# Kernel optimization log

Measured on AMD Instinct MI355X. Metric: run time of the kernel, lower is better.

Reference implementation:

```python
import jax, jax.numpy as jnp
import numpy as np

# Haar (db1) filters after the index reversals done in create_wavelet_filter.
_S = np.float32(1.0 / np.sqrt(2.0))
_LO = np.array([_S, _S], np.float32)
_HI = np.array([_S, -_S], np.float32)
# dec[k, i, j]; band order: LL, (hi rows)*lo, lo*(hi cols), HH -> matches torch stack order
_DEC = np.stack([np.outer(_LO, _LO), np.outer(_HI, _LO), np.outer(_LO, _HI), np.outer(_HI, _HI)], 0)
_REC = _DEC  # identical for Haar


def dwt(x):
    # non-overlapping 2x2 stride-2 depthwise conv == blocked einsum
    b, c, h, w = x.shape
    xr = x.reshape(b, c, h // 2, 2, w // 2, 2)
    return jnp.einsum('bcipjq,kpq->bckij', xr, jnp.asarray(_DEC))  # [b,c,4,h/2,w/2]


def idwt(x):
    # stride-2 kernel-2 transposed depthwise conv == blocked einsum
    b, c, _, h, w = x.shape
    y = jnp.einsum('bckij,kpq->bcipjq', x, jnp.asarray(_REC))
    return y.reshape(b, c, 2 * h, 2 * w)


def dwconv3(x, w, bias=None):
    # depthwise 3x3 'same' conv; w: [C,1,3,3]
    c = x.shape[1]
    y = jax.lax.conv_general_dilated(x, w, (1, 1), 'SAME', feature_group_count=c,
                                     dimension_numbers=('NCHW', 'OIHW', 'NCHW'))
    if bias is not None:
        y = y + bias[None, :, None, None]
    return y


def setup_inputs() -> dict:
    key = jax.random.key(0)
    ks = jax.random.split(key, 8)
    B, C, H, W = 16, 64, 256, 256
    inp = {
        'x': jax.random.normal(ks[0], (B, C, H, W), jnp.float32),
        'base_w': jax.random.normal(ks[1], (C, 1, 3, 3), jnp.float32) * 0.1,
        'base_b': jax.random.normal(ks[2], (C,), jnp.float32) * 0.01,
        'base_scale': jnp.ones((1, C, 1, 1), jnp.float32),
        'ww0': jax.random.normal(ks[3], (4 * C, 1, 3, 3), jnp.float32) * 0.1,
        'ww1': jax.random.normal(ks[4], (4 * C, 1, 3, 3), jnp.float32) * 0.1,
        'ww2': jax.random.normal(ks[5], (4 * C, 1, 3, 3), jnp.float32) * 0.1,
        'ws0': jnp.full((1, 4 * C, 1, 1), 0.1, jnp.float32),
        'ws1': jnp.full((1, 4 * C, 1, 1), 0.1, jnp.float32),
        'ws2': jnp.full((1, 4 * C, 1, 1), 0.1, jnp.float32),
        'gamma': jnp.ones((C,), jnp.float32),
        'beta': jnp.zeros((C,), jnp.float32),
    }
    return inp


def reference(x, base_w, base_b, base_scale, ww0, ww1, ww2, ws0, ws1, ws2, gamma, beta):
    wws = [ww0, ww1, ww2]
    wss = [ws0, ws1, ws2]
    levels = 3
    lls, hs = [], []
    cur = x
    # --- WTConv2d: recursive wavelet pyramid (H,W divisible by 2**levels, no odd-pad) ---
    for i in range(levels):
        cx = dwt(cur)                # [b,c,4,h/2,w/2]
        cur = cx[:, :, 0]            # LL feeds next level
        b_, c_, _, h_, w_ = cx.shape
        t = cx.reshape(b_, c_ * 4, h_, w_)
        t = dwconv3(t, wws[i]) * wss[i]   # depthwise conv (no bias) + learned scale
        t = t.reshape(b_, c_, 4, h_, w_)
        lls.append(t[:, :, 0])
        hs.append(t[:, :, 1:4])
    nxt = jnp.zeros_like(lls[-1])
    for i in range(levels - 1, -1, -1):
        ll = lls[i] + nxt
        cx = jnp.concatenate([ll[:, :, None], hs[i]], axis=2)
        nxt = idwt(cx)
    # base depthwise conv path
    y = dwconv3(x, base_w, base_b) * base_scale + nxt
    # --- BatchNorm2d (training-mode batch stats, eps=1e-5) + ReLU ---
    mean = y.mean(axis=(0, 2, 3), keepdims=True)
    var = ((y - mean) ** 2).mean(axis=(0, 2, 3), keepdims=True)
    y = (y - mean) * jax.lax.rsqrt(var + 1e-5)
    y = y * gamma[None, :, None, None] + beta[None, :, None, None]
    return jax.nn.relu(y)
```

## Files before the change

### kernel.cpp

```cpp
#include <hip/hip_runtime.h>
#include <hip/hip_bf16.h>

#define NB 16
#define NC 64

static __device__ __forceinline__ unsigned short f2bfr(float f) {
    union { float f; unsigned u; } cv; cv.f = f;
    unsigned r = cv.u + 0x7fffu + ((cv.u >> 16) & 1u);
    return (unsigned short)(r >> 16);
}
static __device__ __forceinline__ float bfr2f(unsigned short h) {
    union { unsigned u; float f; } cv; cv.u = ((unsigned)h) << 16;
    return cv.f;
}

template <int H>
static __device__ __forceinline__ void stage_tile(
    const float* __restrict__ src, size_t ibase, int sTop, int sLeft,
    float (*sIn)[72], int tid)
{
#pragma unroll
    for (int i = 0; i < 5; ++i) {
        int idx = i * 256 + tid;
        if (idx < 68 * 16) {
            int r = idx >> 4, c4 = (idx & 15) << 2;
            int gy = sTop + r, gx = sLeft + c4;
            float4 v = make_float4(0.f, 0.f, 0.f, 0.f);
            if ((unsigned)gy < (unsigned)H && (unsigned)gx < (unsigned)H)
                v = *(const float4*)(src + ibase + (size_t)gy * H + gx);
            *(float4*)(&sIn[r][c4]) = v;
        }
    }
    if (tid < 136) {
        int r = tid >> 1, c4 = 64 + ((tid & 1) << 2);
        int gy = sTop + r, gx = sLeft + c4;
        float4 v = make_float4(0.f, 0.f, 0.f, 0.f);
        if ((unsigned)gy < (unsigned)H && (unsigned)gx < (unsigned)H)
            v = *(const float4*)(src + ibase + (size_t)gy * H + gx);
        *(float4*)(&sIn[r][c4]) = v;
    }
}

__global__ __launch_bounds__(256) void ll_kernel(
    const float* __restrict__ in, float* __restrict__ ll)
{
    int t = blockIdx.x * 256 + threadIdx.x;
    int jp  = t & 63;
    int i   = (t >> 6) & 127;
    int img = t >> 13;
    size_t ib = (size_t)img * 65536;
    float4 a = *(const float4*)(in + ib + (size_t)(2 * i) * 256 + 4 * jp);
    float4 b = *(const float4*)(in + ib + (size_t)(2 * i + 1) * 256 + 4 * jp);
    float2 o;
    o.x = 0.5f * (a.x + a.y + b.x + b.y);
    o.y = 0.5f * (a.z + a.w + b.z + b.w);
    *(float2*)(ll + (size_t)img * 16384 + (size_t)i * 128 + 2 * jp) = o;
}

template <int H>
__global__ __launch_bounds__(256) void dwt_conv_kernel(
    const float* __restrict__ in, const float* __restrict__ ww,
    const float* __restrict__ wsc, float* __restrict__ t_out,
    float* __restrict__ curn)
{
    constexpr int H2 = H / 2;
    constexpr int TX = H2 / 32;
    const int tile = blockIdx.x;
    const int c = blockIdx.y, b = blockIdx.z;
    const int ty = tile / TX, tx = tile % TX;
    const int oy0 = ty * 32, ox0 = tx * 32;
    const int tid = threadIdx.x;

    __shared__ float sIn[68][72];

    float w[4][9], sc[4];
#pragma unroll
    for (int k = 0; k < 4; ++k) {
#pragma unroll
        for (int i = 0; i < 9; ++i) w[k][i] = ww[(c * 4 + k) * 9 + i];
        sc[k] = 0.5f * wsc[c * 4 + k];
    }

    const size_t ibase = (size_t)(b * NC + c) * H * H;
    stage_tile<H>(in, ibase, 2 * oy0 - 2, 2 * ox0 - 4, sIn, tid);
    __syncthreads();

    const size_t tbase = (size_t)(b * NC + c) * 4 * H2 * H2;
    const size_t cbase = (size_t)(b * NC + c) * H2 * H2;
    const int qj = tid & 31;
    const int qi0 = tid >> 5;
#pragma unroll
    for (int it = 0; it < 4; ++it) {
        int qi = qi0 + 8 * it;
        float P[6][6];
#pragma unroll
        for (int r = 0; r < 6; ++r) {
            const float2* rp = (const float2*)&sIn[2 * qi + r][2 * qj + 2];
            float2 p0 = rp[0], p1 = rp[1], p2 = rp[2];
            P[r][0] = p0.x; P[r][1] = p0.y; P[r][2] = p1.x;
            P[r][3] = p1.y; P[r][4] = p2.x; P[r][5] = p2.y;
        }
        float kk0 = 0.f, kk1 = 0.f, kk2 = 0.f, kk3 = 0.f, llc = 0.f;
#pragma unroll
        for (int r = 0; r < 3; ++r)
#pragma unroll
            for (int s = 0; s < 3; ++s) {
                float a = P[2*r][2*s],   e = P[2*r][2*s+1];
                float f = P[2*r+1][2*s], g = P[2*r+1][2*s+1];
                float s0 = a + e, s1 = f + g, d0 = a - e, d1 = f - g;
                float b0 = s0 + s1;
                kk0 += w[0][3*r+s] * b0;
                kk1 += w[1][3*r+s] * (s0 - s1);
                kk2 += w[2][3*r+s] * (d0 + d1);
                kk3 += w[3][3*r+s] * (d0 - d1);
                if (r == 1 && s == 1) llc = 0.5f * b0;
            }
        size_t o = (size_t)(oy0 + qi) * H2 + (ox0 + qj);
        t_out[tbase + o]                       = kk0 * sc[0];
        t_out[tbase + (size_t)H2 * H2 + o]     = kk1 * sc[1];
        t_out[tbase + (size_t)2 * H2 * H2 + o] = kk2 * sc[2];
        t_out[tbase + (size_t)3 * H2 * H2 + o] = kk3 * sc[3];
        if (curn) curn[cbase + o] = llc;
    }
}

__global__ __launch_bounds__(256) void idwt_fuse_kernel(
    const float* __restrict__ t1, const float* __restrict__ t2,
    float* __restrict__ nxt1)
{
    int idx = blockIdx.x * 256 + threadIdx.x;
    int j = idx & 63, i = (idx >> 6) & 63, img = idx >> 12;
    size_t t2b = (size_t)img * 4096 + (size_t)(i >> 1) * 32 + (j >> 1);
    float m0 = t2[t2b], m1 = t2[t2b + 1024], m2 = t2[t2b + 2048], m3 = t2[t2b + 3072];
    float a1 = (i & 1) ? -m1 : m1;
    float a2 = (j & 1) ? -m2 : m2;
    float a3 = ((i ^ j) & 1) ? -m3 : m3;
    float nxt2v = 0.5f * (m0 + a1 + a2 + a3);
    size_t t1b = (size_t)img * 16384 + (size_t)i * 64 + j;
    float k0 = t1[t1b] + nxt2v;
    float k1 = t1[t1b + 4096], k2 = t1[t1b + 8192], k3 = t1[t1b + 12288];
    size_t ob = (size_t)img * 16384 + (size_t)(2 * i) * 128 + 2 * j;
    *(float2*)(nxt1 + ob) = make_float2(0.5f * (k0 + k1 + k2 + k3),
                                        0.5f * (k0 + k1 - k2 - k3));
    *(float2*)(nxt1 + ob + 128) = make_float2(0.5f * (k0 - k1 + k2 - k3),
                                              0.5f * (k0 - k1 - k2 + k3));
}

__global__ __launch_bounds__(256) void final_fuse_kernel(
    const float* __restrict__ x, const float* __restrict__ nxt1,
    const float* __restrict__ bw, const float* __restrict__ bb,
    const float* __restrict__ bs, const float* __restrict__ ww0,
    const float* __restrict__ ws0,
    unsigned short* __restrict__ ybf, float2* __restrict__ partials)
{
    const int tile = blockIdx.x, c = blockIdx.y, b = blockIdx.z;
    const int ty = tile >> 2, tx = tile & 3;
    const int oy0 = ty * 64, ox0 = tx * 64;
    const int hy0 = ty * 32, hx0 = tx * 32;
    const int tid = threadIdx.x;

    __shared__ float sIn[68][72];
    __shared__ float rS[256], rQ[256];

    float w[4][9], sc[4], wb[9];
#pragma unroll
    for (int k = 0; k < 4; ++k) {
#pragma unroll
        for (int i = 0; i < 9; ++i) w[k][i] = ww0[(c * 4 + k) * 9 + i];
        sc[k] = 0.25f * ws0[c * 4 + k];
    }
#pragma unroll
    for (int i = 0; i < 9; ++i) wb[i] = bw[c * 9 + i];
    const float scale = bs[c];
    const float bsc = bb[c] * scale;

    const size_t xb = (size_t)(b * NC + c) * 65536;
    stage_tile<256>(x, xb, oy0 - 2, ox0 - 4, sIn, tid);
    __syncthreads();

    const size_t n1b = (size_t)(b * NC + c) * 16384;
    const int qj = tid & 31;
    const int qi0 = tid >> 5;
    float lsum = 0.f, lss = 0.f;
#pragma unroll
    for (int it = 0; it < 4; ++it) {
        int qi = qi0 + 8 * it;
        float P[6][6];
#pragma unroll
        for (int r = 0; r < 6; ++r) {
            const float2* rp = (const float2*)&sIn[2 * qi + r][2 * qj + 2];
            float2 p0 = rp[0], p1 = rp[1], p2 = rp[2];
            P[r][0] = p0.x; P[r][1] = p0.y; P[r][2] = p1.x;
            P[r][3] = p1.y; P[r][4] = p2.x; P[r][5] = p2.y;
        }
        float kk0 = 0.f, kk1 = 0.f, kk2 = 0.f, kk3 = 0.f;
#pragma unroll
        for (int r = 0; r < 3; ++r)
#pragma unroll
            for (int s = 0; s < 3; ++s) {
                float a = P[2*r][2*s],   e = P[2*r][2*s+1];
                float f = P[2*r+1][2*s], g = P[2*r+1][2*s+1];
                float s0 = a + e, s1 = f + g, d0 = a - e, d1 = f - g;
                kk0 += w[0][3*r+s] * (s0 + s1);
                kk1 += w[1][3*r+s] * (s0 - s1);
                kk2 += w[2][3*r+s] * (d0 + d1);
                kk3 += w[3][3*r+s] * (d0 - d1);
            }
        kk0 = kk0 * sc[0] + 0.5f * nxt1[n1b + (size_t)(hy0 + qi) * 128 + (hx0 + qj)];
        kk1 *= sc[1];
        kk2 *= sc[2];
        kk3 *= sc[3];
        float vv[2][2];
        vv[0][0] = kk0 + kk1 + kk2 + kk3;
        vv[0][1] = kk0 + kk1 - kk2 - kk3;
        vv[1][0] = kk0 - kk1 + kk2 - kk3;
        vv[1][1] = kk0 - kk1 - kk2 + kk3;
        int yl = 2 * qi, xl = 2 * qj;
#pragma unroll
        for (int p = 0; p < 2; ++p) {
            unsigned pack = 0;
#pragma unroll
            for (int q = 0; q < 2; ++q) {
                float acc = 0.f;
#pragma unroll
                for (int r = 0; r < 3; ++r)
#pragma unroll
                    for (int s = 0; s < 3; ++s)
                        acc += P[p + r + 1][q + s + 1] * wb[3 * r + s];
                float val = fmaf(acc, scale, bsc) + vv[p][q];
                lsum += val;
                lss = fmaf(val, val, lss);
                pack |= ((unsigned)f2bfr(val)) << (16 * q);
            }
            *(unsigned*)(ybf + xb + (size_t)(oy0 + yl + p) * 256 + (ox0 + xl)) = pack;
        }
    }
    rS[tid] = lsum;
    rQ[tid] = lss;
    __syncthreads();
    for (int off = 128; off > 0; off >>= 1) {
        if (tid < off) { rS[tid] += rS[tid + off]; rQ[tid] += rQ[tid + off]; }
        __syncthreads();
    }
    if (tid == 0)
        partials[c * 256 + b * 16 + tile] = make_float2(rS[0], rQ[0]);
}

__global__ __launch_bounds__(256) void stats_kernel(
    const float2* __restrict__ partials, const float* __restrict__ gamma,
    const float* __restrict__ beta, float2* __restrict__ ab)
{
    const int c = blockIdx.x;
    const int tid = threadIdx.x;
    __shared__ float s1[256], s2[256];
    float2 p = partials[c * 256 + tid];
    s1[tid] = p.x;
    s2[tid] = p.y;
    __syncthreads();
    for (int off = 128; off > 0; off >>= 1) {
        if (tid < off) { s1[tid] += s1[tid + off]; s2[tid] += s2[tid + off]; }
        __syncthreads();
    }
    if (tid == 0) {
        const float N = (float)NB * 65536.0f;
        float mean = s1[0] / N;
        float var = s2[0] / N - mean * mean;
        float inv = rsqrtf(var + 1e-5f);
        float a = gamma[c] * inv;
        ab[c] = make_float2(a, beta[c] - mean * a);
    }
}

__global__ __launch_bounds__(256) void norm_out_kernel(
    const unsigned short* __restrict__ ybf, const float2* __restrict__ ab,
    float* __restrict__ out)
{
    const long total8 = (long)NB * NC * 65536 / 8;
    const long stride = (long)gridDim.x * 256;
    for (long i = blockIdx.x * 256L + threadIdx.x; i < total8; i += stride) {
        long e = i * 8;
        int c = (int)((e >> 16) & (NC - 1));
        float2 s = ab[c];
        uint4 v = *(const uint4*)(ybf + e);
        float4 o0, o1;
        o0.x = fmaxf(fmaf(bfr2f((unsigned short)(v.x & 0xffff)), s.x, s.y), 0.f);
        o0.y = fmaxf(fmaf(bfr2f((unsigned short)(v.x >> 16)),    s.x, s.y), 0.f);
        o0.z = fmaxf(fmaf(bfr2f((unsigned short)(v.y & 0xffff)), s.x, s.y), 0.f);
        o0.w = fmaxf(fmaf(bfr2f((unsigned short)(v.y >> 16)),    s.x, s.y), 0.f);
        o1.x = fmaxf(fmaf(bfr2f((unsigned short)(v.z & 0xffff)), s.x, s.y), 0.f);
        o1.y = fmaxf(fmaf(bfr2f((unsigned short)(v.z >> 16)),    s.x, s.y), 0.f);
        o1.z = fmaxf(fmaf(bfr2f((unsigned short)(v.w & 0xffff)), s.x, s.y), 0.f);
        o1.w = fmaxf(fmaf(bfr2f((unsigned short)(v.w >> 16)),    s.x, s.y), 0.f);
        *(float4*)(out + e) = o0;
        *(float4*)(out + e + 4) = o1;
    }
}

extern "C" void kernel_launch(void* const* d_in, const int* in_sizes, int n_in,
                              void* d_out, int out_size, void* d_ws, size_t ws_size,
                              hipStream_t stream)
{
    const float* x    = (const float*)d_in[0];
    const float* bw   = (const float*)d_in[1];
    const float* bb   = (const float*)d_in[2];
    const float* bs   = (const float*)d_in[3];
    const float* ww0  = (const float*)d_in[4];
    const float* ww1  = (const float*)d_in[5];
    const float* ww2  = (const float*)d_in[6];
    const float* ws0  = (const float*)d_in[7];
    const float* ws1  = (const float*)d_in[8];
    const float* ws2  = (const float*)d_in[9];
    const float* gamma = (const float*)d_in[10];
    const float* beta  = (const float*)d_in[11];

    char* w = (char*)d_ws;
    float* cur1 = (float*)(w);
    float* t1   = (float*)(w + 67108864);
    float* cur2 = (float*)(w + 67108864 + 67108864);
    float* t2   = (float*)(w + 67108864 + 83886080);
    unsigned short* ybf = (unsigned short*)(w + 67108864);
    float2* partials = (float2*)(w + 67108864 + 134217728);
    float2* ab       = (float2*)(w + 67108864 + 134217728 + 131072);
    float* nxt1 = cur1;

    ll_kernel<<<dim3(NB * NC * 128 * 64 / 256), 256, 0, stream>>>(x, cur1);
    dwt_conv_kernel<128><<<dim3(4, NC, NB), 256, 0, stream>>>(cur1, ww1, ws1, t1, cur2);
    dwt_conv_kernel<64><<<dim3(1, NC, NB), 256, 0, stream>>>(cur2, ww2, ws2, t2, nullptr);
    idwt_fuse_kernel<<<dim3(NB * NC * 4096 / 256), 256, 0, stream>>>(t1, t2, nxt1);
    final_fuse_kernel<<<dim3(16, NC, NB), 256, 0, stream>>>(x, nxt1, bw, bb, bs, ww0, ws0, ybf, partials);
    stats_kernel<<<dim3(64), 256, 0, stream>>>(partials, gamma, beta, ab);
    norm_out_kernel<<<dim3(2048), 256, 0, stream>>>(ybf, ab, (float*)d_out);
}
```

Before: 363.6 us.

## Fuse idwt into final kernel, store wavelet bands as bf16, 2x2 register blocking

```diff
diff --git a/kernel.cpp b/kernel.cpp
--- a/kernel.cpp
+++ b/kernel.cpp
@@ -13,11 +13,14 @@
     union { unsigned u; float f; } cv; cv.u = ((unsigned)h) << 16;
     return cv.f;
 }
+static __device__ __forceinline__ unsigned pack2bf(float lo, float hi) {
+    return ((unsigned)f2bfr(lo)) | (((unsigned)f2bfr(hi)) << 16);
+}
 
 template <int H>
 static __device__ __forceinline__ void stage_tile(
     const float* __restrict__ src, size_t ibase, int sTop, int sLeft,
-    float (*sIn)[72], int tid)
+    float (*sIn)[76], int tid)
 {
 #pragma unroll
     for (int i = 0; i < 5; ++i) {
@@ -60,7 +63,7 @@
 template <int H>
 __global__ __launch_bounds__(256) void dwt_conv_kernel(
     const float* __restrict__ in, const float* __restrict__ ww,
-    const float* __restrict__ wsc, float* __restrict__ t_out,
+    const float* __restrict__ wsc, unsigned short* __restrict__ t_out,
     float* __restrict__ curn)
 {
     constexpr int H2 = H / 2;
@@ -70,8 +73,9 @@
     const int ty = tile / TX, tx = tile % TX;
     const int oy0 = ty * 32, ox0 = tx * 32;
     const int tid = threadIdx.x;
-
-    __shared__ float sIn[68][72];
+    const int qi = 2 * (tid >> 4), qj = 2 * (tid & 15);
+
+    __shared__ float sIn[68][76];
 
     float w[4][9], sc[4];
 #pragma unroll
@@ -85,81 +89,87 @@
     stage_tile<H>(in, ibase, 2 * oy0 - 2, 2 * ox0 - 4, sIn, tid);
     __syncthreads();
 
+    float kk[4][4];
+#pragma unroll
+    for (int i = 0; i < 4; ++i)
+#pragma unroll
+        for (int j = 0; j < 4; ++j) kk[i][j] = 0.f;
+    float llc[4];
+
+    const int pr0 = 2 * qi, pc0 = 2 * qj + 2;
+#pragma unroll
+    for (int rp = 0; rp < 4; ++rp) {
+        float xa[8], xb[8];
+#pragma unroll
+        for (int n = 0; n < 4; ++n) {
+            float2 va = *(const float2*)&sIn[pr0 + 2 * rp][pc0 + 2 * n];
+            float2 vb = *(const float2*)&sIn[pr0 + 2 * rp + 1][pc0 + 2 * n];
+            xa[2 * n] = va.x; xa[2 * n + 1] = va.y;
+            xb[2 * n] = vb.x; xb[2 * n + 1] = vb.y;
+        }
+        float D0[4], D1[4], D2[4], D3[4];
+#pragma unroll
+        for (int n = 0; n < 4; ++n) {
+            float a = xa[2 * n], e = xa[2 * n + 1];
+            float f = xb[2 * n], g = xb[2 * n + 1];
+            float s0 = a + e, s1 = f + g, d0 = a - e, d1 = f - g;
+            D0[n] = s0 + s1; D1[n] = s0 - s1;
+            D2[n] = d0 + d1; D3[n] = d0 - d1;
+        }
+#pragma unroll
+        for (int mi = 0; mi < 2; ++mi) {
+            const int r = rp - mi;
+            if (r >= 0 && r <= 2) {
+#pragma unroll
+                for (int mj = 0; mj < 2; ++mj) {
+                    const int m = 2 * mi + mj;
+#pragma unroll
+                    for (int s = 0; s < 3; ++s) {
+                        kk[0][m] = fmaf(w[0][3 * r + s], D0[mj + s], kk[0][m]);
+                        kk[1][m] = fmaf(w[1][3 * r + s], D1[mj + s], kk[1][m]);
+                        kk[2][m] = fmaf(w[2][3 * r + s], D2[mj + s], kk[2][m]);
+                        kk[3][m] = fmaf(w[3][3 * r + s], D3[mj + s], kk[3][m]);
+                    }
+                }
+                if (r == 1) {
+                    llc[2 * mi + 0] = 0.5f * D0[1];
+                    llc[2 * mi + 1] = 0.5f * D0[2];
+                }
+            }
+        }
+    }
+
     const size_t tbase = (size_t)(b * NC + c) * 4 * H2 * H2;
-    const size_t cbase = (size_t)(b * NC + c) * H2 * H2;
-    const int qj = tid & 31;
-    const int qi0 = tid >> 5;
-#pragma unroll
-    for (int it = 0; it < 4; ++it) {
-        int qi = qi0 + 8 * it;
-        float P[6][6];
-#pragma unroll
-        for (int r = 0; r < 6; ++r) {
-            const float2* rp = (const float2*)&sIn[2 * qi + r][2 * qj + 2];
-            float2 p0 = rp[0], p1 = rp[1], p2 = rp[2];
-            P[r][0] = p0.x; P[r][1] = p0.y; P[r][2] = p1.x;
-            P[r][3] = p1.y; P[r][4] = p2.x; P[r][5] = p2.y;
-        }
-        float kk0 = 0.f, kk1 = 0.f, kk2 = 0.f, kk3 = 0.f, llc = 0.f;
-#pragma unroll
-        for (int r = 0; r < 3; ++r)
-#pragma unroll
-            for (int s = 0; s < 3; ++s) {
-                float a = P[2*r][2*s],   e = P[2*r][2*s+1];
-                float f = P[2*r+1][2*s], g = P[2*r+1][2*s+1];
-                float s0 = a + e, s1 = f + g, d0 = a - e, d1 = f - g;
-                float b0 = s0 + s1;
-                kk0 += w[0][3*r+s] * b0;
-                kk1 += w[1][3*r+s] * (s0 - s1);
-                kk2 += w[2][3*r+s] * (d0 + d1);
-                kk3 += w[3][3*r+s] * (d0 - d1);
-                if (r == 1 && s == 1) llc = 0.5f * b0;
-            }
-        size_t o = (size_t)(oy0 + qi) * H2 + (ox0 + qj);
-        t_out[tbase + o]                       = kk0 * sc[0];
-        t_out[tbase + (size_t)H2 * H2 + o]     = kk1 * sc[1];
-        t_out[tbase + (size_t)2 * H2 * H2 + o] = kk2 * sc[2];
-        t_out[tbase + (size_t)3 * H2 * H2 + o] = kk3 * sc[3];
-        if (curn) curn[cbase + o] = llc;
-    }
-}
-
-__global__ __launch_bounds__(256) void idwt_fuse_kernel(
-    const float* __restrict__ t1, const float* __restrict__ t2,
-    float* __restrict__ nxt1)
-{
-    int idx = blockIdx.x * 256 + threadIdx.x;
-    int j = idx & 63, i = (idx >> 6) & 63, img = idx >> 12;
-    size_t t2b = (size_t)img * 4096 + (size_t)(i >> 1) * 32 + (j >> 1);
-    float m0 = t2[t2b], m1 = t2[t2b + 1024], m2 = t2[t2b + 2048], m3 = t2[t2b + 3072];
-    float a1 = (i & 1) ? -m1 : m1;
-    float a2 = (j & 1) ? -m2 : m2;
-    float a3 = ((i ^ j) & 1) ? -m3 : m3;
-    float nxt2v = 0.5f * (m0 + a1 + a2 + a3);
-    size_t t1b = (size_t)img * 16384 + (size_t)i * 64 + j;
-    float k0 = t1[t1b] + nxt2v;
-    float k1 = t1[t1b + 4096], k2 = t1[t1b + 8192], k3 = t1[t1b + 12288];
-    size_t ob = (size_t)img * 16384 + (size_t)(2 * i) * 128 + 2 * j;
-    *(float2*)(nxt1 + ob) = make_float2(0.5f * (k0 + k1 + k2 + k3),
-                                        0.5f * (k0 + k1 - k2 - k3));
-    *(float2*)(nxt1 + ob + 128) = make_float2(0.5f * (k0 - k1 + k2 - k3),
-                                              0.5f * (k0 - k1 - k2 + k3));
+    const size_t o00 = (size_t)(oy0 + qi) * H2 + (ox0 + qj);
+#pragma unroll
+    for (int band = 0; band < 4; ++band) {
+        size_t bo = tbase + (size_t)band * H2 * H2 + o00;
+#pragma unroll
+        for (int mi = 0; mi < 2; ++mi)
+            *(unsigned*)(t_out + bo + (size_t)mi * H2) =
+                pack2bf(kk[band][2 * mi] * sc[band], kk[band][2 * mi + 1] * sc[band]);
+    }
+    if (curn) {
+        const size_t cbase = (size_t)(b * NC + c) * H2 * H2 + o00;
+        *(float2*)(curn + cbase)      = make_float2(llc[0], llc[1]);
+        *(float2*)(curn + cbase + H2) = make_float2(llc[2], llc[3]);
+    }
 }
 
 __global__ __launch_bounds__(256) void final_fuse_kernel(
-    const float* __restrict__ x, const float* __restrict__ nxt1,
-    const float* __restrict__ bw, const float* __restrict__ bb,
-    const float* __restrict__ bs, const float* __restrict__ ww0,
-    const float* __restrict__ ws0,
+    const float* __restrict__ x, const unsigned short* __restrict__ t1,
+    const unsigned short* __restrict__ t2, const float* __restrict__ bw,
+    const float* __restrict__ bb, const float* __restrict__ bs,
+    const float* __restrict__ ww0, const float* __restrict__ ws0,
     unsigned short* __restrict__ ybf, float2* __restrict__ partials)
 {
     const int tile = blockIdx.x, c = blockIdx.y, b = blockIdx.z;
     const int ty = tile >> 2, tx = tile & 3;
     const int oy0 = ty * 64, ox0 = tx * 64;
-    const int hy0 = ty * 32, hx0 = tx * 32;
     const int tid = threadIdx.x;
-
-    __shared__ float sIn[68][72];
+    const int qi = 2 * (tid >> 4), qj = 2 * (tid & 15);
+
+    __shared__ float sIn[68][76];
     __shared__ float rS[256], rQ[256];
 
     float w[4][9], sc[4], wb[9];
@@ -176,65 +186,134 @@
 
     const size_t xb = (size_t)(b * NC + c) * 65536;
     stage_tile<256>(x, xb, oy0 - 2, ox0 - 4, sIn, tid);
+
+    const int i1 = ty * 16 + (tid >> 4);
+    const int j1 = tx * 16 + (tid & 15);
+    const size_t img = (size_t)(b * NC + c);
+    const size_t t1b = img * 16384 + (size_t)i1 * 64 + j1;
+    const size_t t2b = img * 4096 + (size_t)(i1 >> 1) * 32 + (j1 >> 1);
+    float m0 = bfr2f(t2[t2b]);
+    float m1 = bfr2f(t2[t2b + 1024]);
+    float m2 = bfr2f(t2[t2b + 2048]);
+    float m3 = bfr2f(t2[t2b + 3072]);
+    float a1 = (i1 & 1) ? -m1 : m1;
+    float a2 = (j1 & 1) ? -m2 : m2;
+    float a3 = ((i1 ^ j1) & 1) ? -m3 : m3;
+    float k0 = bfr2f(t1[t1b]) + 0.5f * (m0 + a1 + a2 + a3);
+    float k1 = bfr2f(t1[t1b + 4096]);
+    float k2 = bfr2f(t1[t1b + 8192]);
+    float k3 = bfr2f(t1[t1b + 12288]);
+    float nxtq[2][2];
+    nxtq[0][0] = 0.25f * (k0 + k1 + k2 + k3);
+    nxtq[0][1] = 0.25f * (k0 + k1 - k2 - k3);
+    nxtq[1][0] = 0.25f * (k0 - k1 + k2 - k3);
+    nxtq[1][1] = 0.25f * (k0 - k1 - k2 + k3);
+
     __syncthreads();
 
-    const size_t n1b = (size_t)(b * NC + c) * 16384;
-    const int qj = tid & 31;
-    const int qi0 = tid >> 5;
+    float kk[4][4];
+#pragma unroll
+    for (int i = 0; i < 4; ++i)
+#pragma unroll
+        for (int j = 0; j < 4; ++j) kk[i][j] = 0.f;
+    float acc[4][4];
+#pragma unroll
+    for (int i = 0; i < 4; ++i)
+#pragma unroll
+        for (int j = 0; j < 4; ++j) acc[i][j] = 0.f;
+
+    const int pr0 = 2 * qi, pc0 = 2 * qj + 2;
+#pragma unroll
+    for (int rp = 0; rp < 4; ++rp) {
+        float xa[8], xb8[8];
+#pragma unroll
+        for (int n = 0; n < 4; ++n) {
+            float2 va = *(const float2*)&sIn[pr0 + 2 * rp][pc0 + 2 * n];
+            float2 vb = *(const float2*)&sIn[pr0 + 2 * rp + 1][pc0 + 2 * n];
+            xa[2 * n] = va.x; xa[2 * n + 1] = va.y;
+            xb8[2 * n] = vb.x; xb8[2 * n + 1] = vb.y;
+        }
+        float D0[4], D1[4], D2[4], D3[4];
+#pragma unroll
+        for (int n = 0; n < 4; ++n) {
+            float a = xa[2 * n], e = xa[2 * n + 1];
+            float f = xb8[2 * n], g = xb8[2 * n + 1];
+            float s0 = a + e, s1 = f + g, d0 = a - e, d1 = f - g;
+            D0[n] = s0 + s1; D1[n] = s0 - s1;
+            D2[n] = d0 + d1; D3[n] = d0 - d1;
+        }
+#pragma unroll
+        for (int mi = 0; mi < 2; ++mi) {
+            const int r = rp - mi;
+            if (r >= 0 && r <= 2) {
+#pragma unroll
+                for (int mj = 0; mj < 2; ++mj) {
+                    const int m = 2 * mi + mj;
+#pragma unroll
+                    for (int s = 0; s < 3; ++s) {
+                        kk[0][m] = fmaf(w[0][3 * r + s], D0[mj + s], kk[0][m]);
+                        kk[1][m] = fmaf(w[1][3 * r + s], D1[mj + s], kk[1][m]);
+                        kk[2][m] = fmaf(w[2][3 * r + s], D2[mj + s], kk[2][m]);
+                        kk[3][m] = fmaf(w[3][3 * r + s], D3[mj + s], kk[3][m]);
+                    }
+                }
+            }
+        }
+#pragma unroll
+        for (int half = 0; half < 2; ++half) {
+            const int kr = 2 * rp + half;
+#pragma unroll
+            for (int p = 0; p < 4; ++p) {
+                const int rr = kr - 1 - p;
+                if (rr >= 0 && rr < 3) {
+#pragma unroll
+                    for (int u = 0; u < 4; ++u) {
+                        float t = half ? (xb8[u + 1] * wb[3 * rr] +
+                                          xb8[u + 2] * wb[3 * rr + 1] +
+                                          xb8[u + 3] * wb[3 * rr + 2])
+                                       : (xa[u + 1] * wb[3 * rr] +
+                                          xa[u + 2] * wb[3 * rr + 1] +
+                                          xa[u + 3] * wb[3 * rr + 2]);
+                        acc[p][u] += t;
+                    }
+                }
+            }
+        }
+    }
+
+    float val[4][4];
     float lsum = 0.f, lss = 0.f;
 #pragma unroll
-    for (int it = 0; it < 4; ++it) {
-        int qi = qi0 + 8 * it;
-        float P[6][6];
-#pragma unroll
-        for (int r = 0; r < 6; ++r) {
-            const float2* rp = (const float2*)&sIn[2 * qi + r][2 * qj + 2];
-            float2 p0 = rp[0], p1 = rp[1], p2 = rp[2];
-            P[r][0] = p0.x; P[r][1] = p0.y; P[r][2] = p1.x;
-            P[r][3] = p1.y; P[r][4] = p2.x; P[r][5] = p2.y;
-        }
-        float kk0 = 0.f, kk1 = 0.f, kk2 = 0.f, kk3 = 0.f;
-#pragma unroll
-        for (int r = 0; r < 3; ++r)
-#pragma unroll
-            for (int s = 0; s < 3; ++s) {
-                float a = P[2*r][2*s],   e = P[2*r][2*s+1];
-                float f = P[2*r+1][2*s], g = P[2*r+1][2*s+1];
-                float s0 = a + e, s1 = f + g, d0 = a - e, d1 = f - g;
-                kk0 += w[0][3*r+s] * (s0 + s1);
-                kk1 += w[1][3*r+s] * (s0 - s1);
-                kk2 += w[2][3*r+s] * (d0 + d1);
-                kk3 += w[3][3*r+s] * (d0 - d1);
-            }
-        kk0 = kk0 * sc[0] + 0.5f * nxt1[n1b + (size_t)(hy0 + qi) * 128 + (hx0 + qj)];
-        kk1 *= sc[1];
-        kk2 *= sc[2];
-        kk3 *= sc[3];
-        float vv[2][2];
-        vv[0][0] = kk0 + kk1 + kk2 + kk3;
-        vv[0][1] = kk0 + kk1 - kk2 - kk3;
-        vv[1][0] = kk0 - kk1 + kk2 - kk3;
-        vv[1][1] = kk0 - kk1 - kk2 + kk3;
-        int yl = 2 * qi, xl = 2 * qj;
-#pragma unroll
-        for (int p = 0; p < 2; ++p) {
-            unsigned pack = 0;
-#pragma unroll
-            for (int q = 0; q < 2; ++q) {
-                float acc = 0.f;
-#pragma unroll
-                for (int r = 0; r < 3; ++r)
-#pragma unroll
-                    for (int s = 0; s < 3; ++s)
-                        acc += P[p + r + 1][q + s + 1] * wb[3 * r + s];
-                float val = fmaf(acc, scale, bsc) + vv[p][q];
-                lsum += val;
-                lss = fmaf(val, val, lss);
-                pack |= ((unsigned)f2bfr(val)) << (16 * q);
-            }
-            *(unsigned*)(ybf + xb + (size_t)(oy0 + yl + p) * 256 + (ox0 + xl)) = pack;
-        }
-    }
+    for (int mi = 0; mi < 2; ++mi)
+#pragma unroll
+        for (int mj = 0; mj < 2; ++mj) {
+            const int m = 2 * mi + mj;
+            float c0 = fmaf(kk[0][m], sc[0], nxtq[mi][mj]);
+            float c1 = kk[1][m] * sc[1];
+            float c2 = kk[2][m] * sc[2];
+            float c3 = kk[3][m] * sc[3];
+            float vv00 = c0 + c1 + c2 + c3;
+            float vv01 = c0 + c1 - c2 - c3;
+            float vv10 = c0 - c1 + c2 - c3;
+            float vv11 = c0 - c1 - c2 + c3;
+            val[2 * mi + 0][2 * mj + 0] = fmaf(acc[2 * mi + 0][2 * mj + 0], scale, bsc) + vv00;
+            val[2 * mi + 0][2 * mj + 1] = fmaf(acc[2 * mi + 0][2 * mj + 1], scale, bsc) + vv01;
+            val[2 * mi + 1][2 * mj + 0] = fmaf(acc[2 * mi + 1][2 * mj + 0], scale, bsc) + vv10;
+            val[2 * mi + 1][2 * mj + 1] = fmaf(acc[2 * mi + 1][2 * mj + 1], scale, bsc) + vv11;
+        }
+#pragma unroll
+    for (int p = 0; p < 4; ++p) {
+#pragma unroll
+        for (int u = 0; u < 4; ++u) {
+            lsum += val[p][u];
+            lss = fmaf(val[p][u], val[p][u], lss);
+        }
+        uint2 st;
+        st.x = pack2bf(val[p][0], val[p][1]);
+        st.y = pack2bf(val[p][2], val[p][3]);
+        *(uint2*)(ybf + xb + (size_t)(oy0 + 2 * qi + p) * 256 + (ox0 + 2 * qj)) = st;
+    }
+
     rS[tid] = lsum;
     rQ[tid] = lss;
     __syncthreads();
@@ -314,20 +393,18 @@
     const float* beta  = (const float*)d_in[11];
 
     char* w = (char*)d_ws;
-    float* cur1 = (float*)(w);
-    float* t1   = (float*)(w + 67108864);
-    float* cur2 = (float*)(w + 67108864 + 67108864);
-    float* t2   = (float*)(w + 67108864 + 83886080);
-    unsigned short* ybf = (unsigned short*)(w + 67108864);
-    float2* partials = (float2*)(w + 67108864 + 134217728);
-    float2* ab       = (float2*)(w + 67108864 + 134217728 + 131072);
-    float* nxt1 = cur1;
+    unsigned short* ybf = (unsigned short*)(w);
+    float*          cur1 = (float*)(w);
+    unsigned short* t1   = (unsigned short*)(w + 134217728);
+    float*          cur2 = (float*)(w + 167772160);
+    unsigned short* t2   = (unsigned short*)(w + 184549376);
+    float2*         partials = (float2*)(w + 192937984);
+    float2*         ab       = (float2*)(w + 193069056);
 
     ll_kernel<<<dim3(NB * NC * 128 * 64 / 256), 256, 0, stream>>>(x, cur1);
     dwt_conv_kernel<128><<<dim3(4, NC, NB), 256, 0, stream>>>(cur1, ww1, ws1, t1, cur2);
     dwt_conv_kernel<64><<<dim3(1, NC, NB), 256, 0, stream>>>(cur2, ww2, ws2, t2, nullptr);
-    idwt_fuse_kernel<<<dim3(NB * NC * 4096 / 256), 256, 0, stream>>>(t1, t2, nxt1);
-    final_fuse_kernel<<<dim3(16, NC, NB), 256, 0, stream>>>(x, nxt1, bw, bb, bs, ww0, ws0, ybf, partials);
+    final_fuse_kernel<<<dim3(16, NC, NB), 256, 0, stream>>>(x, t1, t2, bw, bb, bs, ww0, ws0, ybf, partials);
     stats_kernel<<<dim3(64), 256, 0, stream>>>(partials, gamma, beta, ab);
     norm_out_kernel<<<dim3(2048), 256, 0, stream>>>(ybf, ab, (float*)d_out);
 }
```

After: 411.2 us. +13.1%, slower.

## Store wavelet intermediates in bf16 and compute 2x2 outputs per thread

Applied to the files above, without the earlier changes.

```diff
diff --git a/kernel.cpp b/kernel.cpp
--- a/kernel.cpp
+++ b/kernel.cpp
@@ -13,11 +13,14 @@
     union { unsigned u; float f; } cv; cv.u = ((unsigned)h) << 16;
     return cv.f;
 }
+static __device__ __forceinline__ unsigned pack2bf(float lo, float hi) {
+    return ((unsigned)f2bfr(lo)) | (((unsigned)f2bfr(hi)) << 16);
+}
 
 template <int H>
 static __device__ __forceinline__ void stage_tile(
     const float* __restrict__ src, size_t ibase, int sTop, int sLeft,
-    float (*sIn)[72], int tid)
+    float (*sIn)[76], int tid)
 {
 #pragma unroll
     for (int i = 0; i < 5; ++i) {
@@ -60,7 +63,7 @@
 template <int H>
 __global__ __launch_bounds__(256) void dwt_conv_kernel(
     const float* __restrict__ in, const float* __restrict__ ww,
-    const float* __restrict__ wsc, float* __restrict__ t_out,
+    const float* __restrict__ wsc, unsigned short* __restrict__ t_out,
     float* __restrict__ curn)
 {
     constexpr int H2 = H / 2;
@@ -70,8 +73,9 @@
     const int ty = tile / TX, tx = tile % TX;
     const int oy0 = ty * 32, ox0 = tx * 32;
     const int tid = threadIdx.x;
-
-    __shared__ float sIn[68][72];
+    const int qi = 2 * (tid >> 4), qj = 2 * (tid & 15);
+
+    __shared__ float sIn[68][76];
 
     float w[4][9], sc[4];
 #pragma unroll
@@ -85,69 +89,102 @@
     stage_tile<H>(in, ibase, 2 * oy0 - 2, 2 * ox0 - 4, sIn, tid);
     __syncthreads();
 
+    float kk[4][4];
+#pragma unroll
+    for (int i = 0; i < 4; ++i)
+#pragma unroll
+        for (int j = 0; j < 4; ++j) kk[i][j] = 0.f;
+    float llc[4];
+
+    const int pr0 = 2 * qi, pc0 = 2 * qj + 2;
+#pragma unroll
+    for (int rp = 0; rp < 4; ++rp) {
+        float xa[8], xb[8];
+#pragma unroll
+        for (int n = 0; n < 4; ++n) {
+            float2 va = *(const float2*)&sIn[pr0 + 2 * rp][pc0 + 2 * n];
+            float2 vb = *(const float2*)&sIn[pr0 + 2 * rp + 1][pc0 + 2 * n];
+            xa[2 * n] = va.x; xa[2 * n + 1] = va.y;
+            xb[2 * n] = vb.x; xb[2 * n + 1] = vb.y;
+        }
+        float D0[4], D1[4], D2[4], D3[4];
+#pragma unroll
+        for (int n = 0; n < 4; ++n) {
+            float a = xa[2 * n], e = xa[2 * n + 1];
+            float f = xb[2 * n], g = xb[2 * n + 1];
+            float s0 = a + e, s1 = f + g, d0 = a - e, d1 = f - g;
+            D0[n] = s0 + s1; D1[n] = s0 - s1;
+            D2[n] = d0 + d1; D3[n] = d0 - d1;
+        }
+#pragma unroll
+        for (int mi = 0; mi < 2; ++mi) {
+            const int r = rp - mi;
+            if (r >= 0 && r <= 2) {
+#pragma unroll
+                for (int mj = 0; mj < 2; ++mj) {
+                    const int m = 2 * mi + mj;
+#pragma unroll
+                    for (int s = 0; s < 3; ++s) {
+                        kk[0][m] = fmaf(w[0][3 * r + s], D0[mj + s], kk[0][m]);
+                        kk[1][m] = fmaf(w[1][3 * r + s], D1[mj + s], kk[1][m]);
+                        kk[2][m] = fmaf(w[2][3 * r + s], D2[mj + s], kk[2][m]);
+                        kk[3][m] = fmaf(w[3][3 * r + s], D3[mj + s], kk[3][m]);
+                    }
+                }
+                if (r == 1) {
+                    llc[2 * mi + 0] = 0.5f * D0[1];
+                    llc[2 * mi + 1] = 0.5f * D0[2];
+                }
+            }
+        }
+    }
+
     const size_t tbase = (size_t)(b * NC + c) * 4 * H2 * H2;
-    const size_t cbase = (size_t)(b * NC + c) * H2 * H2;
-    const int qj = tid & 31;
-    const int qi0 = tid >> 5;
-#pragma unroll
-    for (int it = 0; it < 4; ++it) {
-        int qi = qi0 + 8 * it;
-        float P[6][6];
-#pragma unroll
-        for (int r = 0; r < 6; ++r) {
-            const float2* rp = (const float2*)&sIn[2 * qi + r][2 * qj + 2];
-            float2 p0 = rp[0], p1 = rp[1], p2 = rp[2];
-            P[r][0] = p0.x; P[r][1] = p0.y; P[r][2] = p1.x;
-            P[r][3] = p1.y; P[r][4] = p2.x; P[r][5] = p2.y;
-        }
-        float kk0 = 0.f, kk1 = 0.f, kk2 = 0.f, kk3 = 0.f, llc = 0.f;
-#pragma unroll
-        for (int r = 0; r < 3; ++r)
-#pragma unroll
-            for (int s = 0; s < 3; ++s) {
-                float a = P[2*r][2*s],   e = P[2*r][2*s+1];
-                float f = P[2*r+1][2*s], g = P[2*r+1][2*s+1];
-                float s0 = a + e, s1 = f + g, d0 = a - e, d1 = f - g;
-                float b0 = s0 + s1;
-                kk0 += w[0][3*r+s] * b0;
-                kk1 += w[1][3*r+s] * (s0 - s1);
-                kk2 += w[2][3*r+s] * (d0 + d1);
-                kk3 += w[3][3*r+s] * (d0 - d1);
-                if (r == 1 && s == 1) llc = 0.5f * b0;
-            }
-        size_t o = (size_t)(oy0 + qi) * H2 + (ox0 + qj);
-        t_out[tbase + o]                       = kk0 * sc[0];
-        t_out[tbase + (size_t)H2 * H2 + o]     = kk1 * sc[1];
-        t_out[tbase + (size_t)2 * H2 * H2 + o] = kk2 * sc[2];
-        t_out[tbase + (size_t)3 * H2 * H2 + o] = kk3 * sc[3];
-        if (curn) curn[cbase + o] = llc;
+    const size_t o00 = (size_t)(oy0 + qi) * H2 + (ox0 + qj);
+#pragma unroll
+    for (int band = 0; band < 4; ++band) {
+        size_t bo = tbase + (size_t)band * H2 * H2 + o00;
+#pragma unroll
+        for (int mi = 0; mi < 2; ++mi)
+            *(unsigned*)(t_out + bo + (size_t)mi * H2) =
+                pack2bf(kk[band][2 * mi] * sc[band], kk[band][2 * mi + 1] * sc[band]);
+    }
+    if (curn) {
+        const size_t cbase = (size_t)(b * NC + c) * H2 * H2 + o00;
+        *(float2*)(curn + cbase)      = make_float2(llc[0], llc[1]);
+        *(float2*)(curn + cbase + H2) = make_float2(llc[2], llc[3]);
     }
 }
 
 __global__ __launch_bounds__(256) void idwt_fuse_kernel(
-    const float* __restrict__ t1, const float* __restrict__ t2,
-    float* __restrict__ nxt1)
+    const unsigned short* __restrict__ t1, const unsigned short* __restrict__ t2,
+    unsigned short* __restrict__ nxt1)
 {
     int idx = blockIdx.x * 256 + threadIdx.x;
     int j = idx & 63, i = (idx >> 6) & 63, img = idx >> 12;
     size_t t2b = (size_t)img * 4096 + (size_t)(i >> 1) * 32 + (j >> 1);
-    float m0 = t2[t2b], m1 = t2[t2b + 1024], m2 = t2[t2b + 2048], m3 = t2[t2b + 3072];
+    float m0 = bfr2f(t2[t2b]);
+    float m1 = bfr2f(t2[t2b + 1024]);
+    float m2 = bfr2f(t2[t2b + 2048]);
+    float m3 = bfr2f(t2[t2b + 3072]);
     float a1 = (i & 1) ? -m1 : m1;
     float a2 = (j & 1) ? -m2 : m2;
     float a3 = ((i ^ j) & 1) ? -m3 : m3;
     float nxt2v = 0.5f * (m0 + a1 + a2 + a3);
     size_t t1b = (size_t)img * 16384 + (size_t)i * 64 + j;
-    float k0 = t1[t1b] + nxt2v;
-    float k1 = t1[t1b + 4096], k2 = t1[t1b + 8192], k3 = t1[t1b + 12288];
+    float k0 = bfr2f(t1[t1b]) + nxt2v;
+    float k1 = bfr2f(t1[t1b + 4096]);
+    float k2 = bfr2f(t1[t1b + 8192]);
+    float k3 = bfr2f(t1[t1b + 12288]);
     size_t ob = (size_t)img * 16384 + (size_t)(2 * i) * 128 + 2 * j;
-    *(float2*)(nxt1 + ob) = make_float2(0.5f * (k0 + k1 + k2 + k3),
-                                        0.5f * (k0 + k1 - k2 - k3));
-    *(float2*)(nxt1 + ob + 128) = make_float2(0.5f * (k0 - k1 + k2 - k3),
-                                              0.5f * (k0 - k1 - k2 + k3));
+    *(unsigned*)(nxt1 + ob)       = pack2bf(0.5f * (k0 + k1 + k2 + k3),
+                                            0.5f * (k0 + k1 - k2 - k3));
+    *(unsigned*)(nxt1 + ob + 128) = pack2bf(0.5f * (k0 - k1 + k2 - k3),
+                                            0.5f * (k0 - k1 - k2 + k3));
 }
 
 __global__ __launch_bounds__(256) void final_fuse_kernel(
-    const float* __restrict__ x, const float* __restrict__ nxt1,
+    const float* __restrict__ x, const unsigned short* __restrict__ nxt1,
     const float* __restrict__ bw, const float* __restrict__ bb,
     const float* __restrict__ bs, const float* __restrict__ ww0,
     const float* __restrict__ ws0,
@@ -159,7 +196,7 @@
     const int hy0 = ty * 32, hx0 = tx * 32;
     const int tid = threadIdx.x;
 
-    __shared__ float sIn[68][72];
+    __shared__ float sIn[68][76];
     __shared__ float rS[256], rQ[256];
 
     float w[4][9], sc[4], wb[9];
@@ -206,7 +243,7 @@
                 kk2 += w[2][3*r+s] * (d0 + d1);
                 kk3 += w[3][3*r+s] * (d0 - d1);
             }
-        kk0 = kk0 * sc[0] + 0.5f * nxt1[n1b + (size_t)(hy0 + qi) * 128 + (hx0 + qj)];
+        kk0 = kk0 * sc[0] + 0.5f * bfr2f(nxt1[n1b + (size_t)(hy0 + qi) * 128 + (hx0 + qj)]);
         kk1 *= sc[1];
         kk2 *= sc[2];
         kk3 *= sc[3];
@@ -314,14 +351,14 @@
     const float* beta  = (const float*)d_in[11];
 
     char* w = (char*)d_ws;
-    float* cur1 = (float*)(w);
-    float* t1   = (float*)(w + 67108864);
-    float* cur2 = (float*)(w + 67108864 + 67108864);
-    float* t2   = (float*)(w + 67108864 + 83886080);
-    unsigned short* ybf = (unsigned short*)(w + 67108864);
-    float2* partials = (float2*)(w + 67108864 + 134217728);
-    float2* ab       = (float2*)(w + 67108864 + 134217728 + 131072);
-    float* nxt1 = cur1;
+    unsigned short* ybf  = (unsigned short*)(w);
+    float*          cur1 = (float*)(w);
+    unsigned short* t1   = (unsigned short*)(w + 134217728);
+    float*          cur2 = (float*)(w + 167772160);
+    unsigned short* t2   = (unsigned short*)(w + 184549376);
+    unsigned short* nxt1 = (unsigned short*)(w + 192937984);
+    float2*         partials = (float2*)(w + 226492416);
+    float2*         ab       = (float2*)(w + 226623488);
 
     ll_kernel<<<dim3(NB * NC * 128 * 64 / 256), 256, 0, stream>>>(x, cur1);
     dwt_conv_kernel<128><<<dim3(4, NC, NB), 256, 0, stream>>>(cur1, ww1, ws1, t1, cur2);
```

Result: faster. 347.0 us (-4.6%).
